# Optimization experiments

Measured on AMD Instinct MI355X. Metric: run time of the kernel, lower is better.

The kernel has to match this reference:

```python
import jax, jax.numpy as jnp
import numpy as np

B, S, D, H, F = 4, 2048, 1024, 16, 4096
DH = D // H
EPS = 1e-6


def setup_inputs() -> dict:
    key = jax.random.key(0)
    ks = jax.random.split(key, 8)
    sc = 1.0 / np.sqrt(D)
    return {
        "x": jax.random.normal(ks[0], (B, S, D), jnp.float32),
        "wq": jax.random.normal(ks[1], (D, D), jnp.float32) * sc,
        "bq": jnp.zeros((D,), jnp.float32),
        "wk": jax.random.normal(ks[2], (D, D), jnp.float32) * sc,
        "bk": jnp.zeros((D,), jnp.float32),
        "wv": jax.random.normal(ks[3], (D, D), jnp.float32) * sc,
        "bv": jnp.zeros((D,), jnp.float32),
        "wo": jax.random.normal(ks[4], (D, D), jnp.float32) * sc,
        "bo": jnp.zeros((D,), jnp.float32),
        "w1": jax.random.normal(ks[5], (D, F), jnp.float32) * sc,
        "b1": jnp.zeros((F,), jnp.float32),
        "w2": jax.random.normal(ks[6], (F, D), jnp.float32) * (1.0 / np.sqrt(F)),
        "b2": jnp.zeros((D,), jnp.float32),
        "g1": jnp.ones((D,), jnp.float32),
        "be1": jnp.zeros((D,), jnp.float32),
        "g2": jnp.ones((D,), jnp.float32),
        "be2": jnp.zeros((D,), jnp.float32),
    }


def _layernorm(x, g, b):
    mu = jnp.mean(x, axis=-1, keepdims=True)
    var = jnp.mean(jnp.square(x - mu), axis=-1, keepdims=True)
    return (x - mu) * jax.lax.rsqrt(var + EPS) * g + b


def reference(x, wq, bq, wk, bk, wv, bv, wo, bo, w1, b1, w2, b2, g1, be1, g2, be2):
    # self-attention: q=k=v=x
    q = (x @ wq + bq).reshape(B, S, H, DH).transpose(0, 2, 1, 3)  # [B,H,S,DH]
    k = (x @ wk + bk).reshape(B, S, H, DH).transpose(0, 2, 1, 3)
    v = (x @ wv + bv).reshape(B, S, H, DH).transpose(0, 2, 1, 3)
    logits = jnp.einsum("bhqd,bhkd->bhqk", q, k) / jnp.sqrt(jnp.float32(DH))
    attn = jax.nn.softmax(logits, axis=-1)
    ctx = jnp.einsum("bhqk,bhkd->bhqd", attn, v)  # [B,H,S,DH]
    ctx = ctx.transpose(0, 2, 1, 3).reshape(B, S, D)
    attn_out = ctx @ wo + bo
    out1 = _layernorm(x + attn_out, g1, be1)
    ffn = jax.nn.relu(out1 @ w1 + b1) @ w2 + b2
    out2 = _layernorm(out1 + ffn, g2, be2)
    return out2
```

## Files before the change

kernel.cpp:

```cpp
#include <hip/hip_runtime.h>

typedef unsigned short u16;
typedef unsigned int u32;

typedef __attribute__((ext_vector_type(8))) short short8;
typedef __attribute__((ext_vector_type(4))) float floatx4;
typedef __attribute__((ext_vector_type(16))) float floatx16;
typedef __attribute__((ext_vector_type(2))) unsigned int uint2v;
typedef __attribute__((ext_vector_type(4))) unsigned int uint4v;

static __device__ __forceinline__ u16 f2b(float f) {
    union { float f; u32 i; } v; v.f = f;
    u32 r = v.i + 0x7fffu + ((v.i >> 16) & 1u);
    return (u16)(r >> 16);
}
static __device__ __forceinline__ float exp2f_hw(float x) {
    return __builtin_amdgcn_exp2f(x);
}
static __device__ __forceinline__ u32 cvtpk(float lo, float hi) {
    u32 r;
    asm("v_cvt_pk_bf16_f32 %0, %1, %2" : "=v"(r) : "v"(lo), "v"(hi));
    return r;
}

static __device__ __forceinline__ floatx4 mfma16(short8 a, short8 b, floatx4 c) {
    return __builtin_amdgcn_mfma_f32_16x16x32_bf16(a, b, c, 0, 0, 0);
}
static __device__ __forceinline__ floatx16 mfma32(short8 a, short8 b, floatx16 c) {
    return __builtin_amdgcn_mfma_f32_32x32x16_bf16(a, b, c, 0, 0, 0);
}

typedef __attribute__((address_space(1))) const void gas_void;
typedef __attribute__((address_space(3))) void las_void;
static __device__ __forceinline__ void gl_lds16(const void* g, void* l) {
    __builtin_amdgcn_global_load_lds((gas_void*)g, (las_void*)l, 16, 0, 0);
}

template<int N> static __device__ __forceinline__ void vmw() {
    if constexpr (N == 0)      asm volatile("s_waitcnt vmcnt(0)" ::: "memory");
    else if constexpr (N == 4) asm volatile("s_waitcnt vmcnt(4)" ::: "memory");
}
#define SBAR() asm volatile("s_barrier" ::: "memory")

#define B_ 4
#define S_ 2048
#define D_ 1024
#define H_ 16
#define DH_ 64
#define F_ 4096
#define QKVS 3072

#define QSCALE 0.18033688011112042f

__global__ __launch_bounds__(256) void cast_b(const float* __restrict__ in,
                                              u16* __restrict__ out, int n4) {
    int id = blockIdx.x * 256 + threadIdx.x;
    if (id < n4) {
        float4 v = ((const float4*)in)[id];
        ushort4 u;
        u.x = f2b(v.x); u.y = f2b(v.y); u.z = f2b(v.z); u.w = f2b(v.w);
        ((ushort4*)out)[id] = u;
    }
}

__global__ __launch_bounds__(256) void concat_bias(const float* __restrict__ bq,
                                                   const float* __restrict__ bk,
                                                   const float* __restrict__ bv,
                                                   float* __restrict__ o) {
    int i = blockIdx.x * 256 + threadIdx.x;
    float v;
    if (i < 1024) v = bq[i] * QSCALE;
    else if (i < 2048) v = bk[i - 1024];
    else v = bv[i - 2048];
    o[i] = v;
}

__global__ void transpose_cast(const float* __restrict__ in, u16* __restrict__ out,
                               int R, int C, float scale) {
    __shared__ float t[32][33];
    int bx = blockIdx.x;
    int by = blockIdx.y;
    int x = threadIdx.x, y = threadIdx.y;
#pragma unroll
    for (int i = 0; i < 4; ++i) {
        int r = by * 32 + y + i * 8;
        t[y + i * 8][x] = in[(size_t)r * C + bx * 32 + x];
    }
    __syncthreads();
#pragma unroll
    for (int i = 0; i < 4; ++i) {
        int c = bx * 32 + y + i * 8;
        out[(size_t)c * R + by * 32 + x] = f2b(t[x][y + i * 8] * scale);
    }
}

__global__ void transpose_v(const u16* __restrict__ qkv, u16* __restrict__ vt) {
    __shared__ u16 t[32][33];
    int bh = blockIdx.z; int b = bh >> 4, h = bh & 15;
    int s0 = blockIdx.x * 32, d0 = blockIdx.y * 32;
    int x = threadIdx.x, y = threadIdx.y;
#pragma unroll
    for (int i = 0; i < 4; ++i)
        t[y + i * 8][x] =
            qkv[(size_t)(b * S_ + s0 + y + i * 8) * QKVS + 2048 + h * DH_ + d0 + x];
    __syncthreads();
#pragma unroll
    for (int i = 0; i < 4; ++i)
        vt[((size_t)bh * DH_ + d0 + y + i * 8) * S_ + s0 + x] = t[x][y + i * 8];
}

#define MFMA16X(MH)                                                        \
    __builtin_amdgcn_s_setprio(1);                                         \
    acc[(MH)*4+0][0] = mfma16(af0, bf0, acc[(MH)*4+0][0]);                 \
    acc[(MH)*4+0][1] = mfma16(af0, bf1, acc[(MH)*4+0][1]);                 \
    acc[(MH)*4+0][2] = mfma16(af0, bf2, acc[(MH)*4+0][2]);                 \
    acc[(MH)*4+0][3] = mfma16(af0, bf3, acc[(MH)*4+0][3]);                 \
    acc[(MH)*4+1][0] = mfma16(af1, bf0, acc[(MH)*4+1][0]);                 \
    acc[(MH)*4+1][1] = mfma16(af1, bf1, acc[(MH)*4+1][1]);                 \
    acc[(MH)*4+1][2] = mfma16(af1, bf2, acc[(MH)*4+1][2]);                 \
    acc[(MH)*4+1][3] = mfma16(af1, bf3, acc[(MH)*4+1][3]);                 \
    acc[(MH)*4+2][0] = mfma16(af2, bf0, acc[(MH)*4+2][0]);                 \
    acc[(MH)*4+2][1] = mfma16(af2, bf1, acc[(MH)*4+2][1]);                 \
    acc[(MH)*4+2][2] = mfma16(af2, bf2, acc[(MH)*4+2][2]);                 \
    acc[(MH)*4+2][3] = mfma16(af2, bf3, acc[(MH)*4+2][3]);                 \
    acc[(MH)*4+3][0] = mfma16(af3, bf0, acc[(MH)*4+3][0]);                 \
    acc[(MH)*4+3][1] = mfma16(af3, bf1, acc[(MH)*4+3][1]);                 \
    acc[(MH)*4+3][2] = mfma16(af3, bf2, acc[(MH)*4+3][2]);                 \
    acc[(MH)*4+3][3] = mfma16(af3, bf3, acc[(MH)*4+3][3]);                 \
    __builtin_amdgcn_s_setprio(0);

#define PPAIR(P, KH, ST0, W0, ST1, W1) {                                   \
    int ro = l * 64 + ((((KH) * 4 + quad) ^ l7) << 3);                     \
    const u16* bBp = &smem[32768 + (P) * 16384 + wc * 4096];               \
    short8 bf0 = *(const short8*)&bBp[ro];                                 \
    short8 bf1 = *(const short8*)&bBp[ro + 1024];                          \
    short8 bf2 = *(const short8*)&bBp[ro + 2048];                          \
    short8 bf3 = *(const short8*)&bBp[ro + 3072];                          \
    {   const u16* bAp = &smem[(P) * 16384 + (wr * 2 + 0) * 4096];         \
        short8 af0 = *(const short8*)&bAp[ro];                             \
        short8 af1 = *(const short8*)&bAp[ro + 1024];                      \
        short8 af2 = *(const short8*)&bAp[ro + 2048];                      \
        short8 af3 = *(const short8*)&bAp[ro + 3072];                      \
        ST0; W0; SBAR();                                                   \
        MFMA16X(0)                                                         \
        SBAR();                                                            \
    }                                                                      \
    {   const u16* bAp = &smem[(P) * 16384 + (wr * 2 + 1) * 4096];         \
        short8 af0 = *(const short8*)&bAp[ro];                             \
        short8 af1 = *(const short8*)&bAp[ro + 1024];                      \
        short8 af2 = *(const short8*)&bAp[ro + 2048];                      \
        short8 af3 = *(const short8*)&bAp[ro + 3072];                      \
        ST1; W1; SBAR();                                                   \
        MFMA16X(1)                                                         \
        SBAR();                                                            \
    } }

__global__ __launch_bounds__(512) void gemm256(const u16* __restrict__ A,
                                               const u16* __restrict__ Bt,
                                               const float* __restrict__ bias,
                                               float* __restrict__ outF,
                                               float* __restrict__ outF2,
                                               u16* __restrict__ outB,
                                               int M, int N, int K, int klen,
                                               int relu) {
    __shared__ __align__(16) u16 smem[65536];

    int tid = threadIdx.x;
    int w = tid >> 6, lane = tid & 63, quad = lane >> 4, l = lane & 15;
    int wr = w >> 2, wc = w & 3;
    int l7 = l & 7;

    int nbN = gridDim.x, nwg = gridDim.x * gridDim.y;
    int flat = blockIdx.y * gridDim.x + blockIdx.x;
    int swz = (flat & 7) * (nwg >> 3) + (flat >> 3);
    int bM = swz / nbN, bN = swz % nbN;
    int koff = blockIdx.z * klen;

    floatx4 acc[8][4];
#pragma unroll
    for (int i = 0; i < 8; ++i)
#pragma unroll
        for (int j = 0; j < 4; ++j) acc[i][j] = (floatx4){0.f, 0.f, 0.f, 0.f};

    int rT = tid >> 3, cT = tid & 7;
    int cg8 = ((cT ^ (rT & 7)) << 3);
    const u16* gA0 = A + (size_t)(bM * 256 + rT) * K + koff + cg8;
    const u16* gB0 = Bt + (size_t)(bN * 256 + rT) * K + koff + cg8;

    auto stA = [&](int p, int ch, int t) {
        gl_lds16(gA0 + (size_t)(ch * 64) * K + t * 64,
                 (void*)&smem[p * 16384 + ch * 4096 + (w << 9)]);
    };
    auto stB = [&](int p, int hb, int t) {
        gl_lds16(gB0 + (size_t)(hb * 64) * K + t * 64,
                 (void*)&smem[32768 + p * 16384 + hb * 4096 + (w << 9)]);
    };

    stA(0, 0, 0); stA(0, 1, 0); stA(0, 2, 0); stA(0, 3, 0);
    stB(0, 0, 0); stB(0, 1, 0); stB(0, 2, 0); stB(0, 3, 0);
    stA(1, 0, 1); stA(1, 2, 1); stB(1, 0, 1); stB(1, 1, 1);
    vmw<4>(); SBAR();

    const int NI = klen >> 7;
    for (int i = 0; i < NI - 1; ++i) {
        int t1 = 2 * i + 1, t2 = 2 * i + 2, t3 = 2 * i + 3;
        PPAIR(0, 0, (stA(1,1,t1), stA(1,3,t1), stB(1,2,t1), stB(1,3,t1)),
                    ((void)0), ((void)0), ((void)0))
        PPAIR(0, 1, ((void)0), ((void)0),
                    (stA(0,0,t2), stA(0,2,t2), stB(0,0,t2), stB(0,1,t2)), vmw<4>())
        PPAIR(1, 0, (stA(0,1,t2), stA(0,3,t2), stB(0,2,t2), stB(0,3,t2)),
                    ((void)0), ((void)0), ((void)0))
        PPAIR(1, 1, ((void)0), ((void)0),
                    (stA(1,0,t3), stA(1,2,t3), stB(1,0,t3), stB(1,1,t3)), vmw<4>())
    }
    {
        int t1 = 2 * (NI - 1) + 1;
        PPAIR(0, 0, (stA(1,1,t1), stA(1,3,t1), stB(1,2,t1), stB(1,3,t1)),
                    ((void)0), ((void)0), ((void)0))
        PPAIR(0, 1, ((void)0), ((void)0), ((void)0), vmw<0>())
        PPAIR(1, 0, ((void)0), ((void)0), ((void)0), ((void)0))
        PPAIR(1, 1, ((void)0), ((void)0), ((void)0), ((void)0))
    }

    float* of = (blockIdx.z == 0) ? outF : outF2;
    const float* bp = (blockIdx.z == 0) ? bias : nullptr;
    float bv4[4];
#pragma unroll
    for (int nt = 0; nt < 4; ++nt) {
        int colg = bN * 256 + wc * 64 + nt * 16 + l;
        bv4[nt] = bp ? bp[colg] : 0.f;
    }
#pragma unroll
    for (int mt = 0; mt < 8; ++mt) {
#pragma unroll
        for (int rr = 0; rr < 4; ++rr) {
            int rowg = bM * 256 + wr * 128 + mt * 16 + quad * 4 + rr;
            size_t rb = (size_t)rowg * N + bN * 256 + wc * 64 + l;
#pragma unroll
            for (int nt = 0; nt < 4; ++nt) {
                float v = acc[mt][nt][rr] + bv4[nt];
                if (relu) v = fmaxf(v, 0.f);
                if (of) of[rb + nt * 16] = v;
                if (outB) outB[rb + nt * 16] = f2b(v);
            }
        }
    }
}

#define PACK8(sv, rb, dst) {                                                   \
    u32 pa_ = cvtpk(sv[rb + 0], sv[rb + 1]), pb_ = cvtpk(sv[rb + 4], sv[rb + 5]); \
    u32 pc_ = cvtpk(sv[rb + 2], sv[rb + 3]), pd_ = cvtpk(sv[rb + 6], sv[rb + 7]); \
    uint2v t0_ = __builtin_amdgcn_permlane32_swap(pa_, pb_, 0, 0);             \
    uint2v t1_ = __builtin_amdgcn_permlane32_swap(pc_, pd_, 0, 0);             \
    union { uint4v u; short8 s8; } cv_;                                        \
    cv_.u = (uint4v){t0_[0], t1_[0], t0_[1], t1_[1]};                          \
    dst = cv_.s8; }

__global__ __launch_bounds__(256, 4) void attn_kernel(const u16* __restrict__ qkv,
                                                      const u16* __restrict__ vt,
                                                      u16* __restrict__ ctx) {
    __shared__ __align__(16) u16 Kb[2][64 * 64];
    __shared__ __align__(16) u16 Vb[2][64 * 64];

    int bh = blockIdx.x; int b = bh >> 4, h = bh & 15;
    int tid = threadIdx.x;
    int w = tid >> 6, lane = tid & 63;
    int l32 = lane & 31, hi = lane >> 5, row7 = lane & 7;
    int qw = blockIdx.y * 128 + w * 32;

    int r = lane >> 3, c = lane & 7;
    int cs = ((c ^ r) << 3);
    const u16* gK0 = qkv + (size_t)(b * S_ + w * 16 + r) * QKVS + 1024 + h * DH_ + cs;
    const u16* gK1 = gK0 + (size_t)8 * QKVS;
    const u16* gV0 = vt + (size_t)(bh * DH_ + w * 16 + r) * S_ + cs;
    const u16* gV1 = gV0 + (size_t)8 * S_;

    auto stage = [&](int bb) {
        u16* lk = &Kb[bb][w * 16 * 64];
        u16* lv = &Vb[bb][w * 16 * 64];
        gl_lds16(gK0, lk);
        gl_lds16(gK1, lk + 8 * 64);
        gl_lds16(gV0, lv);
        gl_lds16(gV1, lv + 8 * 64);
        gK0 += (size_t)64 * QKVS; gK1 += (size_t)64 * QKVS;
        gV0 += 64; gV1 += 64;
    };

    short8 qf0, qf1, qf2, qf3;
    {
        const u16* qp = qkv + (size_t)(b * S_ + qw + l32) * QKVS + h * DH_ + hi * 8;
        qf0 = *(const short8*)(qp);
        qf1 = *(const short8*)(qp + 16);
        qf2 = *(const short8*)(qp + 32);
        qf3 = *(const short8*)(qp + 48);
    }

    floatx16 O0, O1;
#pragma unroll
    for (int i = 0; i < 16; ++i) { O0[i] = 0.f; O1[i] = 0.f; }
    float lra = 0.f, lrb = 0.f, lrc = 0.f, lrd = 0.f;

    int roff0 = l32 * 64;
    int roff1 = (32 + l32) * 64;

    stage(0);
    __syncthreads();

    const int NT = S_ / 64;
    for (int kt = 0; kt < NT; ++kt) {
        int cur = kt & 1;
        if (kt + 1 < NT) stage(cur ^ 1);

        const u16* Kc = Kb[cur];
        const u16* Vc = Vb[cur];

        floatx16 s0;
#pragma unroll
        for (int i = 0; i < 16; ++i) s0[i] = 0.f;
#pragma unroll
        for (int kc = 0; kc < 4; ++kc) {
            int ch = (((kc * 2 + hi) ^ row7) << 3);
            short8 ka = *(const short8*)&Kc[roff0 + ch];
            short8 qk = (kc == 0) ? qf0 : (kc == 1) ? qf1 : (kc == 2) ? qf2 : qf3;
            s0 = mfma32(ka, qk, s0);
        }
#pragma unroll
        for (int i = 0; i < 16; ++i) s0[i] = exp2f_hw(s0[i]);
        short8 pa0, pa1;
        PACK8(s0, 0, pa0);
        PACK8(s0, 8, pa1);

        floatx16 s1;
#pragma unroll
        for (int i = 0; i < 16; ++i) s1[i] = 0.f;
#pragma unroll
        for (int kc = 0; kc < 4; ++kc) {
            int ch = (((kc * 2 + hi) ^ row7) << 3);
            short8 ka = *(const short8*)&Kc[roff1 + ch];
            short8 qk = (kc == 0) ? qf0 : (kc == 1) ? qf1 : (kc == 2) ? qf2 : qf3;
            s1 = mfma32(ka, qk, s1);
        }
#pragma unroll
        for (int i = 0; i < 16; ++i) s1[i] = exp2f_hw(s1[i]);
        short8 pa2, pa3;
        PACK8(s1, 0, pa2);
        PACK8(s1, 8, pa3);

#pragma unroll
        for (int i = 0; i < 16; i += 4) {
            lra += s0[i + 0] + s1[i + 0];
            lrb += s0[i + 1] + s1[i + 1];
            lrc += s0[i + 2] + s1[i + 2];
            lrd += s0[i + 3] + s1[i + 3];
        }

        {
            short8 vb0 = *(const short8*)&Vc[roff0 + (((0 + hi) ^ row7) << 3)];
            O0 = mfma32(pa0, vb0, O0);
            short8 vb1 = *(const short8*)&Vc[roff0 + (((2 + hi) ^ row7) << 3)];
            O0 = mfma32(pa1, vb1, O0);
            short8 vb2 = *(const short8*)&Vc[roff0 + (((4 + hi) ^ row7) << 3)];
            O0 = mfma32(pa2, vb2, O0);
            short8 vb3 = *(const short8*)&Vc[roff0 + (((6 + hi) ^ row7) << 3)];
            O0 = mfma32(pa3, vb3, O0);
        }
        {
            short8 vb0 = *(const short8*)&Vc[roff1 + (((0 + hi) ^ row7) << 3)];
            O1 = mfma32(pa0, vb0, O1);
            short8 vb1 = *(const short8*)&Vc[roff1 + (((2 + hi) ^ row7) << 3)];
            O1 = mfma32(pa1, vb1, O1);
            short8 vb2 = *(const short8*)&Vc[roff1 + (((4 + hi) ^ row7) << 3)];
            O1 = mfma32(pa2, vb2, O1);
            short8 vb3 = *(const short8*)&Vc[roff1 + (((6 + hi) ^ row7) << 3)];
            O1 = mfma32(pa3, vb3, O1);
        }

        __syncthreads();
    }

    float lr = (lra + lrb) + (lrc + lrd);
    lr += __shfl_xor(lr, 32);
    float inv = 1.0f / lr;
#pragma unroll
    for (int rr = 0; rr < 16; ++rr) {
        int rowq = (rr & 3) + 8 * (rr >> 2) + 4 * hi;
        float iv = __shfl(inv, rowq);
        size_t base = (size_t)(b * S_ + qw + rowq) * D_ + h * DH_ + l32;
        ctx[base]      = f2b(O0[rr] * iv);
        ctx[base + 32] = f2b(O1[rr] * iv);
    }
}

__global__ __launch_bounds__(256) void add_ln(const float* __restrict__ a,
                                              const float* __restrict__ b,
                                              const float* __restrict__ g,
                                              const float* __restrict__ be,
                                              float* __restrict__ outF,
                                              u16* __restrict__ outB) {
    int row = blockIdx.x, tid = threadIdx.x;
    size_t base = (size_t)row * D_;
    float4 va = ((const float4*)(a + base))[tid];
    float4 vb = ((const float4*)(b + base))[tid];
    float x0 = va.x + vb.x, x1 = va.y + vb.y, x2 = va.z + vb.z, x3 = va.w + vb.w;
    float s1 = x0 + x1 + x2 + x3;
    float s2 = x0 * x0 + x1 * x1 + x2 * x2 + x3 * x3;
#pragma unroll
    for (int off = 32; off; off >>= 1) {
        s1 += __shfl_xor(s1, off);
        s2 += __shfl_xor(s2, off);
    }
    __shared__ float r1[4], r2[4];
    int w = tid >> 6, lane = tid & 63;
    if (lane == 0) { r1[w] = s1; r2[w] = s2; }
    __syncthreads();
    s1 = r1[0] + r1[1] + r1[2] + r1[3];
    s2 = r2[0] + r2[1] + r2[2] + r2[3];
    float mean = s1 * (1.0f / D_);
    float var = s2 * (1.0f / D_) - mean * mean;
    float inv = rsqrtf(var + 1e-6f);
    float4 vg = ((const float4*)g)[tid];
    float4 vbe = ((const float4*)be)[tid];
    float o0 = (x0 - mean) * inv * vg.x + vbe.x;
    float o1 = (x1 - mean) * inv * vg.y + vbe.y;
    float o2 = (x2 - mean) * inv * vg.z + vbe.z;
    float o3 = (x3 - mean) * inv * vg.w + vbe.w;
    float4 o; o.x = o0; o.y = o1; o.z = o2; o.w = o3;
    ((float4*)(outF + base))[tid] = o;
    if (outB) {
        ushort4 u;
        u.x = f2b(o0); u.y = f2b(o1); u.z = f2b(o2); u.w = f2b(o3);
        ((ushort4*)(outB + base))[tid] = u;
    }
}

__global__ __launch_bounds__(256) void add_ln3(const float* __restrict__ a,
                                               const float* __restrict__ b,
                                               const float* __restrict__ c,
                                               const float* __restrict__ g,
                                               const float* __restrict__ be,
                                               float* __restrict__ outF,
                                               u16* __restrict__ outB) {
    int row = blockIdx.x, tid = threadIdx.x;
    size_t base = (size_t)row * D_;
    float4 va = ((const float4*)(a + base))[tid];
    float4 vb = ((const float4*)(b + base))[tid];
    float4 vc = ((const float4*)(c + base))[tid];
    float x0 = va.x + vb.x + vc.x, x1 = va.y + vb.y + vc.y;
    float x2 = va.z + vb.z + vc.z, x3 = va.w + vb.w + vc.w;
    float s1 = x0 + x1 + x2 + x3;
    float s2 = x0 * x0 + x1 * x1 + x2 * x2 + x3 * x3;
#pragma unroll
    for (int off = 32; off; off >>= 1) {
        s1 += __shfl_xor(s1, off);
        s2 += __shfl_xor(s2, off);
    }
    __shared__ float r1[4], r2[4];
    int w = tid >> 6, lane = tid & 63;
    if (lane == 0) { r1[w] = s1; r2[w] = s2; }
    __syncthreads();
    s1 = r1[0] + r1[1] + r1[2] + r1[3];
    s2 = r2[0] + r2[1] + r2[2] + r2[3];
    float mean = s1 * (1.0f / D_);
    float var = s2 * (1.0f / D_) - mean * mean;
    float inv = rsqrtf(var + 1e-6f);
    float4 vg = ((const float4*)g)[tid];
    float4 vbe = ((const float4*)be)[tid];
    float o0 = (x0 - mean) * inv * vg.x + vbe.x;
    float o1 = (x1 - mean) * inv * vg.y + vbe.y;
    float o2 = (x2 - mean) * inv * vg.z + vbe.z;
    float o3 = (x3 - mean) * inv * vg.w + vbe.w;
    float4 o; o.x = o0; o.y = o1; o.z = o2; o.w = o3;
    ((float4*)(outF + base))[tid] = o;
    if (outB) {
        ushort4 u;
        u.x = f2b(o0); u.y = f2b(o1); u.z = f2b(o2); u.w = f2b(o3);
        ((ushort4*)(outB + base))[tid] = u;
    }
}

extern "C" void kernel_launch(void* const* d_in, const int* in_sizes, int n_in,
                              void* d_out, int out_size, void* d_ws, size_t ws_size,
                              hipStream_t stream) {
    const float* x   = (const float*)d_in[0];
    const float* wq  = (const float*)d_in[1];
    const float* bq  = (const float*)d_in[2];
    const float* wk  = (const float*)d_in[3];
    const float* bk  = (const float*)d_in[4];
    const float* wv  = (const float*)d_in[5];
    const float* bv  = (const float*)d_in[6];
    const float* wo  = (const float*)d_in[7];
    const float* bo  = (const float*)d_in[8];
    const float* w1  = (const float*)d_in[9];
    const float* b1  = (const float*)d_in[10];
    const float* w2  = (const float*)d_in[11];
    const float* b2  = (const float*)d_in[12];
    const float* g1  = (const float*)d_in[13];
    const float* be1 = (const float*)d_in[14];
    const float* g2  = (const float*)d_in[15];
    const float* be2 = (const float*)d_in[16];
    float* out = (float*)d_out;
    char* ws = (char*)d_ws;
    const size_t MB = 1u << 20;

    u16* xb      = (u16*)(ws + 0);
    u16* wqkvT   = (u16*)(ws + 16 * MB);
    u16* woT     = (u16*)(ws + 22 * MB);
    u16* w1T     = (u16*)(ws + 24 * MB);
    u16* w2T     = (u16*)(ws + 32 * MB);
    float* qkvb  = (float*)(ws + 40 * MB);
    u16* qkv     = (u16*)(ws + 41 * MB);
    u16* vtb     = (u16*)(ws + 89 * MB);
    u16* ctxb    = (u16*)(ws + 105 * MB);
    float* attn_out = (float*)(ws + 121 * MB);
    float* out1     = (float*)(ws + 153 * MB);
    u16* out1b   = (u16*)(ws + 0);
    float* woP1  = (float*)(ws + 41 * MB);
    u16* hidden  = (u16*)(ws + 41 * MB);
    float* ffn2p0 = (float*)(ws + 121 * MB);

    dim3 tb(32, 8);

    cast_b<<<8192, 256, 0, stream>>>(x, xb, (B_ * S_ * D_) / 4);
    transpose_cast<<<dim3(32, 32), tb, 0, stream>>>(wq, wqkvT, D_, D_, QSCALE);
    transpose_cast<<<dim3(32, 32), tb, 0, stream>>>(wk, wqkvT + 1024 * 1024, D_, D_, 1.0f);
    transpose_cast<<<dim3(32, 32), tb, 0, stream>>>(wv, wqkvT + 2048 * 1024, D_, D_, 1.0f);
    transpose_cast<<<dim3(32, 32), tb, 0, stream>>>(wo, woT, D_, D_, 1.0f);
    transpose_cast<<<dim3(128, 32), tb, 0, stream>>>(w1, w1T, D_, F_, 1.0f);
    transpose_cast<<<dim3(32, 128), tb, 0, stream>>>(w2, w2T, F_, D_, 1.0f);
    concat_bias<<<12, 256, 0, stream>>>(bq, bk, bv, qkvb);

    gemm256<<<dim3(12, 32, 1), 512, 0, stream>>>(xb, wqkvT, qkvb, nullptr, nullptr,
                                                 qkv, B_ * S_, QKVS, D_, D_, 0);
    transpose_v<<<dim3(S_ / 32, DH_ / 32, B_ * H_), tb, 0, stream>>>(qkv, vtb);

    attn_kernel<<<dim3(B_ * H_, S_ / 128), 256, 0, stream>>>(qkv, vtb, ctxb);

    gemm256<<<dim3(4, 32, 2), 512, 0, stream>>>(ctxb, woT, bo, attn_out, woP1,
                                                nullptr, B_ * S_, D_, D_, D_ / 2, 0);
    add_ln3<<<B_ * S_, 256, 0, stream>>>(x, attn_out, woP1, g1, be1, out1, out1b);

    gemm256<<<dim3(16, 32, 1), 512, 0, stream>>>(out1b, w1T, b1, nullptr, nullptr,
                                                 hidden, B_ * S_, F_, D_, D_, 1);
    gemm256<<<dim3(4, 32, 2), 512, 0, stream>>>(hidden, w2T, b2, ffn2p0, out,
                                                nullptr, B_ * S_, D_, F_, F_ / 2, 0);
    add_ln3<<<B_ * S_, 256, 0, stream>>>(out1, ffn2p0, out, g2, be2, out, nullptr);
}
```

Baseline: 523.2 us.

## Process 64 query rows per wave in attention to reuse K/V LDS loads

Each attention wave now handles two 32-row query tiles instead of one, so every K and V fragment read from LDS feeds two MFMAs. The block covers 256 query rows, the grid's y dimension is halved, and launch bounds drop to 2 blocks per SM to allow more registers. This cuts LDS read traffic and K/V staging per query row. In exchange it doubles accumulator and Q register use, lowers occupancy, and halves the number of blocks, which may leave fewer waves to hide latency.

```diff
diff --git a/kernel.cpp b/kernel.cpp
--- a/kernel.cpp
+++ b/kernel.cpp
@@ -256,7 +256,7 @@
     cv_.u = (uint4v){t0_[0], t1_[0], t0_[1], t1_[1]};                          \
     dst = cv_.s8; }
 
-__global__ __launch_bounds__(256, 4) void attn_kernel(const u16* __restrict__ qkv,
+__global__ __launch_bounds__(256, 2) void attn_kernel(const u16* __restrict__ qkv,
                                                       const u16* __restrict__ vt,
                                                       u16* __restrict__ ctx) {
     __shared__ __align__(16) u16 Kb[2][64 * 64];
@@ -266,7 +266,7 @@
     int tid = threadIdx.x;
     int w = tid >> 6, lane = tid & 63;
     int l32 = lane & 31, hi = lane >> 5, row7 = lane & 7;
-    int qw = blockIdx.y * 128 + w * 32;
+    int qw = blockIdx.y * 256 + w * 64;
 
     int r = lane >> 3, c = lane & 7;
     int cs = ((c ^ r) << 3);
@@ -286,19 +286,24 @@
         gV0 += 64; gV1 += 64;
     };
 
-    short8 qf0, qf1, qf2, qf3;
+    short8 qa0, qa1, qa2, qa3, qb0, qb1, qb2, qb3;
     {
-        const u16* qp = qkv + (size_t)(b * S_ + qw + l32) * QKVS + h * DH_ + hi * 8;
-        qf0 = *(const short8*)(qp);
-        qf1 = *(const short8*)(qp + 16);
-        qf2 = *(const short8*)(qp + 32);
-        qf3 = *(const short8*)(qp + 48);
-    }
-
-    floatx16 O0, O1;
-#pragma unroll
-    for (int i = 0; i < 16; ++i) { O0[i] = 0.f; O1[i] = 0.f; }
-    float lra = 0.f, lrb = 0.f, lrc = 0.f, lrd = 0.f;
+        const u16* qpA = qkv + (size_t)(b * S_ + qw + l32) * QKVS + h * DH_ + hi * 8;
+        qa0 = *(const short8*)(qpA);
+        qa1 = *(const short8*)(qpA + 16);
+        qa2 = *(const short8*)(qpA + 32);
+        qa3 = *(const short8*)(qpA + 48);
+        const u16* qpB = qpA + (size_t)32 * QKVS;
+        qb0 = *(const short8*)(qpB);
+        qb1 = *(const short8*)(qpB + 16);
+        qb2 = *(const short8*)(qpB + 32);
+        qb3 = *(const short8*)(qpB + 48);
+    }
+
+    floatx16 OA0, OA1, OB0, OB1;
+#pragma unroll
+    for (int i = 0; i < 16; ++i) { OA0[i] = 0.f; OA1[i] = 0.f; OB0[i] = 0.f; OB1[i] = 0.f; }
+    float lra0 = 0.f, lra1 = 0.f, lrb0 = 0.f, lrb1 = 0.f;
 
     int roff0 = l32 * 64;
     int roff1 = (32 + l32) * 64;
@@ -314,80 +319,109 @@
         const u16* Kc = Kb[cur];
         const u16* Vc = Vb[cur];
 
-        floatx16 s0;
-#pragma unroll
-        for (int i = 0; i < 16; ++i) s0[i] = 0.f;
-#pragma unroll
-        for (int kc = 0; kc < 4; ++kc) {
-            int ch = (((kc * 2 + hi) ^ row7) << 3);
-            short8 ka = *(const short8*)&Kc[roff0 + ch];
-            short8 qk = (kc == 0) ? qf0 : (kc == 1) ? qf1 : (kc == 2) ? qf2 : qf3;
-            s0 = mfma32(ka, qk, s0);
+        short8 paA0, paA1, paA2, paA3, paB0, paB1, paB2, paB3;
+
+        {
+            floatx16 sA, sB;
+#pragma unroll
+            for (int i = 0; i < 16; ++i) { sA[i] = 0.f; sB[i] = 0.f; }
+#pragma unroll
+            for (int kc = 0; kc < 4; ++kc) {
+                int ch = (((kc * 2 + hi) ^ row7) << 3);
+                short8 ka = *(const short8*)&Kc[roff0 + ch];
+                short8 qkA = (kc == 0) ? qa0 : (kc == 1) ? qa1 : (kc == 2) ? qa2 : qa3;
+                short8 qkB = (kc == 0) ? qb0 : (kc == 1) ? qb1 : (kc == 2) ? qb2 : qb3;
+                sA = mfma32(ka, qkA, sA);
+                sB = mfma32(ka, qkB, sB);
+            }
+#pragma unroll
+            for (int i = 0; i < 16; ++i) { sA[i] = exp2f_hw(sA[i]); sB[i] = exp2f_hw(sB[i]); }
+#pragma unroll
+            for (int i = 0; i < 16; i += 4) {
+                lra0 += sA[i + 0] + sA[i + 1];
+                lra1 += sA[i + 2] + sA[i + 3];
+                lrb0 += sB[i + 0] + sB[i + 1];
+                lrb1 += sB[i + 2] + sB[i + 3];
+            }
+            PACK8(sA, 0, paA0); PACK8(sA, 8, paA1);
+            PACK8(sB, 0, paB0); PACK8(sB, 8, paB1);
         }
-#pragma unroll
-        for (int i = 0; i < 16; ++i) s0[i] = exp2f_hw(s0[i]);
-        short8 pa0, pa1;
-        PACK8(s0, 0, pa0);
-        PACK8(s0, 8, pa1);
-
-        floatx16 s1;
-#pragma unroll
-        for (int i = 0; i < 16; ++i) s1[i] = 0.f;
-#pragma unroll
-        for (int kc = 0; kc < 4; ++kc) {
-            int ch = (((kc * 2 + hi) ^ row7) << 3);
-            short8 ka = *(const short8*)&Kc[roff1 + ch];
-            short8 qk = (kc == 0) ? qf0 : (kc == 1) ? qf1 : (kc == 2) ? qf2 : qf3;
-            s1 = mfma32(ka, qk, s1);
-        }
-#pragma unroll
-        for (int i = 0; i < 16; ++i) s1[i] = exp2f_hw(s1[i]);
-        short8 pa2, pa3;
-        PACK8(s1, 0, pa2);
-        PACK8(s1, 8, pa3);
-
-#pragma unroll
-        for (int i = 0; i < 16; i += 4) {
-            lra += s0[i + 0] + s1[i + 0];
-            lrb += s0[i + 1] + s1[i + 1];
-            lrc += s0[i + 2] + s1[i + 2];
-            lrd += s0[i + 3] + s1[i + 3];
+
+        {
+            floatx16 sA, sB;
+#pragma unroll
+            for (int i = 0; i < 16; ++i) { sA[i] = 0.f; sB[i] = 0.f; }
+#pragma unroll
+            for (int kc = 0; kc < 4; ++kc) {
+                int ch = (((kc * 2 + hi) ^ row7) << 3);
+                short8 ka = *(const short8*)&Kc[roff1 + ch];
+                short8 qkA = (kc == 0) ? qa0 : (kc == 1) ? qa1 : (kc == 2) ? qa2 : qa3;
+                short8 qkB = (kc == 0) ? qb0 : (kc == 1) ? qb1 : (kc == 2) ? qb2 : qb3;
+                sA = mfma32(ka, qkA, sA);
+                sB = mfma32(ka, qkB, sB);
+            }
+#pragma unroll
+            for (int i = 0; i < 16; ++i) { sA[i] = exp2f_hw(sA[i]); sB[i] = exp2f_hw(sB[i]); }
+#pragma unroll
+            for (int i = 0; i < 16; i += 4) {
+                lra0 += sA[i + 0] + sA[i + 1];
+                lra1 += sA[i + 2] + sA[i + 3];
+                lrb0 += sB[i + 0] + sB[i + 1];
+                lrb1 += sB[i + 2] + sB[i + 3];
+            }
+            PACK8(sA, 0, paA2); PACK8(sA, 8, paA3);
+            PACK8(sB, 0, paB2); PACK8(sB, 8, paB3);
         }
 
         {
             short8 vb0 = *(const short8*)&Vc[roff0 + (((0 + hi) ^ row7) << 3)];
-            O0 = mfma32(pa0, vb0, O0);
+            OA0 = mfma32(paA0, vb0, OA0);
+            OB0 = mfma32(paB0, vb0, OB0);
             short8 vb1 = *(const short8*)&Vc[roff0 + (((2 + hi) ^ row7) << 3)];
-            O0 = mfma32(pa1, vb1, O0);
+            OA0 = mfma32(paA1, vb1, OA0);
+            OB0 = mfma32(paB1, vb1, OB0);
             short8 vb2 = *(const short8*)&Vc[roff0 + (((4 + hi) ^ row7) << 3)];
-            O0 = mfma32(pa2, vb2, O0);
+            OA0 = mfma32(paA2, vb2, OA0);
+            OB0 = mfma32(paB2, vb2, OB0);
             short8 vb3 = *(const short8*)&Vc[roff0 + (((6 + hi) ^ row7) << 3)];
-            O0 = mfma32(pa3, vb3, O0);
+            OA0 = mfma32(paA3, vb3, OA0);
+            OB0 = mfma32(paB3, vb3, OB0);
         }
         {
             short8 vb0 = *(const short8*)&Vc[roff1 + (((0 + hi) ^ row7) << 3)];
-            O1 = mfma32(pa0, vb0, O1);
+            OA1 = mfma32(paA0, vb0, OA1);
+            OB1 = mfma32(paB0, vb0, OB1);
             short8 vb1 = *(const short8*)&Vc[roff1 + (((2 + hi) ^ row7) << 3)];
-            O1 = mfma32(pa1, vb1, O1);
+            OA1 = mfma32(paA1, vb1, OA1);
+            OB1 = mfma32(paB1, vb1, OB1);
             short8 vb2 = *(const short8*)&Vc[roff1 + (((4 + hi) ^ row7) << 3)];
-            O1 = mfma32(pa2, vb2, O1);
+            OA1 = mfma32(paA2, vb2, OA1);
+            OB1 = mfma32(paB2, vb2, OB1);
             short8 vb3 = *(const short8*)&Vc[roff1 + (((6 + hi) ^ row7) << 3)];
-            O1 = mfma32(pa3, vb3, O1);
+            OA1 = mfma32(paA3, vb3, OA1);
+            OB1 = mfma32(paB3, vb3, OB1);
         }
 
         __syncthreads();
     }
 
-    float lr = (lra + lrb) + (lrc + lrd);
-    lr += __shfl_xor(lr, 32);
-    float inv = 1.0f / lr;
+    float lrA = lra0 + lra1;
+    float lrB = lrb0 + lrb1;
+    lrA += __shfl_xor(lrA, 32);
+    lrB += __shfl_xor(lrB, 32);
+    float invA = 1.0f / lrA;
+    float invB = 1.0f / lrB;
 #pragma unroll
     for (int rr = 0; rr < 16; ++rr) {
         int rowq = (rr & 3) + 8 * (rr >> 2) + 4 * hi;
-        float iv = __shfl(inv, rowq);
-        size_t base = (size_t)(b * S_ + qw + rowq) * D_ + h * DH_ + l32;
-        ctx[base]      = f2b(O0[rr] * iv);
-        ctx[base + 32] = f2b(O1[rr] * iv);
+        float ivA = __shfl(invA, rowq);
+        float ivB = __shfl(invB, rowq);
+        size_t baseA = (size_t)(b * S_ + qw + rowq) * D_ + h * DH_ + l32;
+        ctx[baseA]      = f2b(OA0[rr] * ivA);
+        ctx[baseA + 32] = f2b(OA1[rr] * ivA);
+        size_t baseB = baseA + (size_t)32 * D_;
+        ctx[baseB]      = f2b(OB0[rr] * ivB);
+        ctx[baseB + 32] = f2b(OB1[rr] * ivB);
     }
 }
 
@@ -533,7 +567,7 @@
                                                  qkv, B_ * S_, QKVS, D_, D_, 0);
     transpose_v<<<dim3(S_ / 32, DH_ / 32, B_ * H_), tb, 0, stream>>>(qkv, vtb);
 
-    attn_kernel<<<dim3(B_ * H_, S_ / 128), 256, 0, stream>>>(qkv, vtb, ctxb);
+    attn_kernel<<<dim3(B_ * H_, S_ / 256), 256, 0, stream>>>(qkv, vtb, ctxb);
 
     gemm256<<<dim3(4, 32, 2), 512, 0, stream>>>(ctxb, woT, bo, attn_out, woP1,
                                                 nullptr, B_ * S_, D_, D_, D_ / 2, 0);
```

Result: faster. 505.9 us (-3.3%).
